# Kernel optimization log

Measured on AMD Instinct MI355X. Metric: run time of the kernel, lower is better.

## Reference

```python
import jax, jax.numpy as jnp
import numpy as np

N, D, NUM_CLASSES = 4096, 512, 128
MARGIN = 0.3


def setup_inputs() -> dict:
    key = jax.random.key(0)
    k1, k2 = jax.random.split(key)
    embeddings = jax.random.normal(k1, (N, D), dtype=jnp.float32)
    labels = jax.random.randint(k2, (N,), 0, NUM_CLASSES, dtype=jnp.int64)
    return {"embeddings": embeddings, "labels": labels}


def _batch_hard_triplet(embeddings, labels, margin):
    # L2-normalize rows (torch F.normalize: x / max(||x||, eps))
    norm = jnp.linalg.norm(embeddings, axis=1, keepdims=True)
    e = embeddings / jnp.maximum(norm, 1e-12)
    n = e.shape[0]
    # Pairwise Euclidean distance via Gram matrix; ||a-b||^2 = 2 - 2 a.b for unit vectors
    gram = e @ e.T                                   # [N, N]
    sq = jnp.clip(2.0 - 2.0 * gram, 0.0, None)
    # safe sqrt: zero (and exactly-equal) pairs get distance 0 with zero gradient
    nz = sq > 0
    dist = jnp.where(nz, jnp.sqrt(jnp.where(nz, sq, 1.0)), 0.0)  # [N, N]

    same = labels[:, None] == labels[None, :]        # [N, N] bool
    eye = jnp.eye(n, dtype=bool)
    pos_mask = same & ~eye                           # positives excluding self
    neg_mask = ~same

    # hardest positive (row max over positives), hardest negative (row min over negatives)
    dist_ap = jnp.max(jnp.where(pos_mask, dist, -jnp.inf), axis=1)  # [N]
    dist_an = jnp.min(jnp.where(neg_mask, dist, jnp.inf), axis=1)   # [N]

    valid = jnp.any(pos_mask, axis=1) & jnp.any(neg_mask, axis=1)   # rows kept by torch loop
    per_row = jax.nn.relu(dist_ap - dist_an + margin)
    num_valid = jnp.sum(valid)
    loss_sum = jnp.sum(jnp.where(valid, per_row, 0.0))
    return jnp.where(num_valid > 0, loss_sum / jnp.maximum(num_valid, 1), 0.0)


def reference(embeddings, labels):
    return _batch_hard_triplet(embeddings, labels, MARGIN)
```

## Files before the change

### kernel.cpp

```cpp
#include <hip/hip_runtime.h>
#include <hip/hip_bf16.h>
#include <stdint.h>


#define NROW 4096
#define DIM  512
#define MARGIN 0.3f
#define BT 128
#define NTILE (NROW / BT)
#define NPAIR (NTILE * (NTILE + 1) / 2)
#define POS_INIT 0xFFFFFFFFu
#define NEG_INIT 0u

typedef __attribute__((ext_vector_type(8))) __bf16 bf16x8;
typedef __attribute__((ext_vector_type(4))) float  f32x4;
typedef __attribute__((ext_vector_type(8))) unsigned short u16x8;

__device__ __forceinline__ unsigned enc(float f) {
    unsigned u = __float_as_uint(f);
    return (u & 0x80000000u) ? ~u : (u | 0x80000000u);
}
__device__ __forceinline__ float dec(unsigned e) {
    return (e & 0x80000000u) ? __uint_as_float(e & 0x7fffffffu)
                             : __uint_as_float(~e);
}

__device__ __forceinline__ unsigned short f2bf(float f) {
    __hip_bfloat16 h = __float2bfloat16(f);
    return *reinterpret_cast<unsigned short*>(&h);
}

__global__ void tl_norm(const float* __restrict__ E,
                        __hip_bfloat16* __restrict__ Ebf,
                        unsigned* __restrict__ posArr,
                        unsigned* __restrict__ negArr) {
    if (blockIdx.x < 16) {
        int t = blockIdx.x * 256 + threadIdx.x;
        posArr[t] = POS_INIT;
        negArr[t] = NEG_INIT;
    }
    const int wave  = threadIdx.x >> 6;
    const int lane  = threadIdx.x & 63;
    const int r2    = lane >> 4;
    const int kc    = lane & 15;
    const int rtile = blockIdx.x;
    const int r_in  = wave * 4 + r2;
    const int row   = rtile * 16 + r_in;

    const float4* src = (const float4*)(E + (size_t)row * DIM) + kc * 8;
    float4 v[8];
    #pragma unroll
    for (int i = 0; i < 8; i++) v[i] = src[i];

    float ss = 0.0f;
    #pragma unroll
    for (int i = 0; i < 8; i++)
        ss += v[i].x*v[i].x + v[i].y*v[i].y + v[i].z*v[i].z + v[i].w*v[i].w;
    #pragma unroll
    for (int m = 1; m < 16; m <<= 1) ss += __shfl_xor(ss, m);
    const float inv = 1.0f / fmaxf(sqrtf(ss), 1e-12f);

    u16x8* dst = (u16x8*)Ebf + (size_t)kc * 16384 + (size_t)rtile * 64 + r_in;
    #pragma unroll
    for (int c = 0; c < 4; c++) {
        const float4 lo = v[2*c], hi = v[2*c + 1];
        u16x8 o;
        o[0] = f2bf(lo.x * inv); o[1] = f2bf(lo.y * inv);
        o[2] = f2bf(lo.z * inv); o[3] = f2bf(lo.w * inv);
        o[4] = f2bf(hi.x * inv); o[5] = f2bf(hi.y * inv);
        o[6] = f2bf(hi.z * inv); o[7] = f2bf(hi.w * inv);
        dst[c * 16] = o;
    }
}

#define ISSUE8(sl, kkq) do {                                                  \
    const uint4* _pa = EaU + (size_t)(kkq) * 16384;                           \
    const uint4* _pb = EbU + (size_t)(kkq) * 16384;                           \
    asm volatile(                                                             \
        "global_load_dwordx4 %0, %8, off\n\t"                                 \
        "global_load_dwordx4 %1, %8, off offset:1024\n\t"                     \
        "global_load_dwordx4 %2, %8, off offset:2048\n\t"                     \
        "global_load_dwordx4 %3, %8, off offset:3072\n\t"                     \
        "global_load_dwordx4 %4, %9, off\n\t"                                 \
        "global_load_dwordx4 %5, %9, off offset:1024\n\t"                     \
        "global_load_dwordx4 %6, %9, off offset:2048\n\t"                     \
        "global_load_dwordx4 %7, %9, off offset:3072"                         \
        : "=&v"(a[sl][0]), "=&v"(a[sl][1]), "=&v"(a[sl][2]), "=&v"(a[sl][3]), \
          "=&v"(b[sl][0]), "=&v"(b[sl][1]), "=&v"(b[sl][2]), "=&v"(b[sl][3])  \
        : "v"(_pa), "v"(_pb));                                                \
} while (0)

#define WAITV(n) do {                                                         \
    asm volatile("s_waitcnt vmcnt(" #n ")" ::: "memory");                     \
    __builtin_amdgcn_sched_barrier(0);                                        \
} while (0)

#define MFMA16(sl) do {                                                       \
    _Pragma("unroll")                                                         \
    for (int mi = 0; mi < 4; mi++)                                            \
        _Pragma("unroll")                                                     \
        for (int ni = 0; ni < 4; ni++)                                        \
            acc[mi][ni] = __builtin_amdgcn_mfma_f32_16x16x32_bf16(            \
                a[sl][mi], b[sl][ni], acc[mi][ni], 0, 0, 0);                  \
} while (0)

__global__ void __launch_bounds__(256, 2)
tl_gram(const __hip_bfloat16* __restrict__ Ebf,
        const int* __restrict__ labels,
        unsigned* __restrict__ posArr,
        unsigned* __restrict__ negArr) {
    __shared__ int rowLab[BT];
    __shared__ int colLab[BT];

    const int bid = blockIdx.x;
    int t = (bid & 7) * (NPAIR / 8) + (bid >> 3);

    int bi = 0, rowlen = NTILE;
    while (t >= rowlen) { t -= rowlen; rowlen--; bi++; }
    const int bj = bi + t;

    const int tid  = threadIdx.x;
    const int wave = tid >> 6;
    const int lane = tid & 63;
    const int quad = lane >> 4;
    const int l16  = lane & 15;
    const int wr   = wave >> 1;
    const int wc   = wave & 1;
    const int tileI = bi * BT;
    const int tileJ = bj * BT;
    const bool diag = (bi == bj);

    if (tid < BT) rowLab[tid] = labels[tileI + tid];
    else          colLab[tid - BT] = labels[tileJ + (tid - BT)];
    __syncthreads();

    const uint4* Ev  = (const uint4*)Ebf;
    const uint4* EaU = Ev + ((tileI + wr * 64) >> 4) * 64 + lane;
    const uint4* EbU = Ev + ((tileJ + wc * 64) >> 4) * 64 + lane;

    f32x4 acc[4][4] = {};
    bf16x8 a[4][4], b[4][4];

    ISSUE8(0, 0); ISSUE8(1, 1); ISSUE8(2, 2);

    ISSUE8(3, 3);   WAITV(24); MFMA16(0);
    ISSUE8(0, 4);   WAITV(24); MFMA16(1);
    ISSUE8(1, 5);   WAITV(24); MFMA16(2);
    ISSUE8(2, 6);   WAITV(24); MFMA16(3);
    ISSUE8(3, 7);   WAITV(24); MFMA16(0);
    ISSUE8(0, 8);   WAITV(24); MFMA16(1);
    ISSUE8(1, 9);   WAITV(24); MFMA16(2);
    ISSUE8(2, 10);  WAITV(24); MFMA16(3);
    ISSUE8(3, 11);  WAITV(24); MFMA16(0);
    ISSUE8(0, 12);  WAITV(24); MFMA16(1);
    ISSUE8(1, 13);  WAITV(24); MFMA16(2);
    ISSUE8(2, 14);  WAITV(24); MFMA16(3);
    ISSUE8(3, 15);  WAITV(24); MFMA16(0);
                    WAITV(16); MFMA16(1);
                    WAITV(8);  MFMA16(2);
                    WAITV(0);  MFMA16(3);

    int rl[16], cl[4], clocv[4];
    #pragma unroll
    for (int mi = 0; mi < 4; mi++)
        #pragma unroll
        for (int reg = 0; reg < 4; reg++)
            rl[mi * 4 + reg] = rowLab[wr * 64 + mi * 16 + quad * 4 + reg];
    #pragma unroll
    for (int ni = 0; ni < 4; ni++) {
        clocv[ni] = wc * 64 + ni * 16 + l16;
        cl[ni] = colLab[clocv[ni]];
    }

    #pragma unroll
    for (int mi = 0; mi < 4; mi++) {
        #pragma unroll
        for (int reg = 0; reg < 4; reg++) {
            const int rloc = wr * 64 + mi * 16 + quad * 4 + reg;
            const int lr   = rl[mi * 4 + reg];
            const int gi   = tileI + rloc;
            float pmin =  INFINITY;
            float nmax = -INFINITY;
            #pragma unroll
            for (int ni = 0; ni < 4; ni++) {
                const int gj  = tileJ + clocv[ni];
                const float g = acc[mi][ni][reg];
                const bool same = (lr == cl[ni]);
                if (same && gi != gj) pmin = fminf(pmin, g);
                if (!same)            nmax = fmaxf(nmax, g);
            }
            #pragma unroll
            for (int m = 1; m < 16; m <<= 1) {
                pmin = fminf(pmin, __shfl_xor(pmin, m));
                nmax = fmaxf(nmax, __shfl_xor(nmax, m));
            }
            if (l16 == 0) {
                if (pmin <  INFINITY) atomicMin(&posArr[gi], enc(pmin));
                if (nmax > -INFINITY) atomicMax(&negArr[gi], enc(nmax));
            }
        }
    }

    if (!diag) {
        #pragma unroll
        for (int ni = 0; ni < 4; ni++) {
            const int lc = cl[ni];
            const int gj = tileJ + clocv[ni];
            float pmin =  INFINITY;
            float nmax = -INFINITY;
            #pragma unroll
            for (int mi = 0; mi < 4; mi++) {
                #pragma unroll
                for (int reg = 0; reg < 4; reg++) {
                    const float g = acc[mi][ni][reg];
                    const bool same = (rl[mi * 4 + reg] == lc);
                    if (same) pmin = fminf(pmin, g);
                    else      nmax = fmaxf(nmax, g);
                }
            }
            pmin = fminf(pmin, __shfl_xor(pmin, 16));
            pmin = fminf(pmin, __shfl_xor(pmin, 32));
            nmax = fmaxf(nmax, __shfl_xor(nmax, 16));
            nmax = fmaxf(nmax, __shfl_xor(nmax, 32));
            if (quad == 0) {
                if (pmin <  INFINITY) atomicMin(&posArr[gj], enc(pmin));
                if (nmax > -INFINITY) atomicMax(&negArr[gj], enc(nmax));
            }
        }
    }
}

__global__ void tl_final(const unsigned* __restrict__ posArr,
                         const unsigned* __restrict__ negArr,
                         float* __restrict__ out) {
    const int tid = threadIdx.x;
    uint4 pe4 = ((const uint4*)posArr)[tid];
    uint4 ne4 = ((const uint4*)negArr)[tid];
    unsigned pes[4] = {pe4.x, pe4.y, pe4.z, pe4.w};
    unsigned nes[4] = {ne4.x, ne4.y, ne4.z, ne4.w};
    float sum = 0.0f;
    int   count = 0;
    #pragma unroll
    for (int j = 0; j < 4; j++) {
        const bool valid = (pes[j] != POS_INIT) && (nes[j] != NEG_INIT);
        const float dap = sqrtf(fmaxf(2.0f - 2.0f * dec(pes[j]), 0.0f));
        const float dan = sqrtf(fmaxf(2.0f - 2.0f * dec(nes[j]), 0.0f));
        const float per = fmaxf(dap - dan + MARGIN, 0.0f);
        if (valid) { sum += per; count += 1; }
    }
    #pragma unroll
    for (int m = 32; m >= 1; m >>= 1) {
        sum   += __shfl_xor(sum, m);
        count += __shfl_xor(count, m);
    }
    __shared__ float ssum[16];
    __shared__ int   scnt[16];
    const int wave = tid >> 6, lane = tid & 63;
    if (lane == 0) { ssum[wave] = sum; scnt[wave] = count; }
    __syncthreads();
    if (tid == 0) {
        float s = 0.0f; int c = 0;
        #pragma unroll
        for (int w = 0; w < 16; w++) { s += ssum[w]; c += scnt[w]; }
        out[0] = (c > 0) ? (s / (float)c) : 0.0f;
    }
}

extern "C" void kernel_launch(void* const* d_in, const int* in_sizes, int n_in,
                              void* d_out, int out_size, void* d_ws, size_t ws_size,
                              hipStream_t stream) {
    const float* E      = (const float*)d_in[0];
    const int*   labels = (const int*)d_in[1];
    float*       out    = (float*)d_out;

    char* ws = (char*)d_ws;
    __hip_bfloat16* Ebf   = (__hip_bfloat16*)ws;
    unsigned* posArr      = (unsigned*)(ws + (size_t)NROW * DIM * 2);
    unsigned* negArr      = posArr + NROW;

    tl_norm<<<NROW / 16, 256, 0, stream>>>(E, Ebf, posArr, negArr);
    tl_gram<<<NPAIR, 256, 0, stream>>>(Ebf, labels, posArr, negArr);
    tl_final<<<1, 1024, 0, stream>>>(posArr, negArr, out);
}
```

Baseline: 94.98 us.

## Stage Gram operand tiles through LDS via async global-to-LDS loads

Replaces the per-wave direct global-to-register loads with a block-cooperative global_load_lds copy into a 4-stage shared-memory ring. Each K-slice of the row and column tiles is loaded once per block and read by waves with ds_read_b128. This removes the duplicate global loads where waves sharing a row or column tile each fetched it, and it frees the VGPRs that held prefetched operands. In exchange it adds two block barriers per K step and LDS read latency before each MFMA group.

```diff
diff --git a/kernel.cpp b/kernel.cpp
--- a/kernel.cpp
+++ b/kernel.cpp
@@ -30,6 +30,13 @@
     return *reinterpret_cast<unsigned short*>(&h);
 }
 
+__device__ __forceinline__ void async_copy16(const void* g, void* l) {
+    __builtin_amdgcn_global_load_lds(
+        (const __attribute__((address_space(1))) unsigned int*)g,
+        (__attribute__((address_space(3))) unsigned int*)l,
+        16, 0, 0);
+}
+
 __global__ void tl_norm(const float* __restrict__ E,
                         __hip_bfloat16* __restrict__ Ebf,
                         unsigned* __restrict__ posArr,
@@ -73,21 +80,18 @@
     }
 }
 
-#define ISSUE8(sl, kkq) do {                                                  \
-    const uint4* _pa = EaU + (size_t)(kkq) * 16384;                           \
-    const uint4* _pb = EbU + (size_t)(kkq) * 16384;                           \
-    asm volatile(                                                             \
-        "global_load_dwordx4 %0, %8, off\n\t"                                 \
-        "global_load_dwordx4 %1, %8, off offset:1024\n\t"                     \
-        "global_load_dwordx4 %2, %8, off offset:2048\n\t"                     \
-        "global_load_dwordx4 %3, %8, off offset:3072\n\t"                     \
-        "global_load_dwordx4 %4, %9, off\n\t"                                 \
-        "global_load_dwordx4 %5, %9, off offset:1024\n\t"                     \
-        "global_load_dwordx4 %6, %9, off offset:2048\n\t"                     \
-        "global_load_dwordx4 %7, %9, off offset:3072"                         \
-        : "=&v"(a[sl][0]), "=&v"(a[sl][1]), "=&v"(a[sl][2]), "=&v"(a[sl][3]), \
-          "=&v"(b[sl][0]), "=&v"(b[sl][1]), "=&v"(b[sl][2]), "=&v"(b[sl][3])  \
-        : "v"(_pa), "v"(_pb));                                                \
+#define ISSUE(s) do {                                                         \
+    if ((s) < 16) {                                                           \
+        _Pragma("unroll")                                                     \
+        for (int q = 0; q < 4; ++q) {                                         \
+            const int c   = wave * 4 + q;                                     \
+            const int rt0 = (c >= 8) ? rtJ0 : rtI0;                           \
+            const int rt  = (c >= 8) ? c - 8 : c;                             \
+            const uint4* src = Ev + (size_t)(s) * 16384                       \
+                                  + (size_t)(rt0 + rt) * 64 + lane;           \
+            async_copy16(src, &sbuf[(s) & 3][c][0]);                          \
+        }                                                                     \
+    }                                                                         \
 } while (0)
 
 #define WAITV(n) do {                                                         \
@@ -95,13 +99,34 @@
     __builtin_amdgcn_sched_barrier(0);                                        \
 } while (0)
 
-#define MFMA16(sl) do {                                                       \
+#define DSR(dst, addr) \
+    asm volatile("ds_read_b128 %0, %1" : "=&v"(dst) : "v"(addr));
+
+#define COMPUTE(s) do {                                                       \
+    bf16x8 af[4], bg[4];                                                      \
+    _Pragma("unroll")                                                         \
+    for (int mi = 0; mi < 4; mi++)                                            \
+        DSR(af[mi], vA + (unsigned)(((s) & 3) * 16384 + mi * 1024));          \
+    _Pragma("unroll")                                                         \
+    for (int ni = 0; ni < 4; ni++)                                            \
+        DSR(bg[ni], vB + (unsigned)(((s) & 3) * 16384 + ni * 1024));          \
+    asm volatile("s_waitcnt lgkmcnt(0)" ::: "memory");                        \
+    __builtin_amdgcn_sched_barrier(0);                                        \
     _Pragma("unroll")                                                         \
     for (int mi = 0; mi < 4; mi++)                                            \
         _Pragma("unroll")                                                     \
         for (int ni = 0; ni < 4; ni++)                                        \
             acc[mi][ni] = __builtin_amdgcn_mfma_f32_16x16x32_bf16(            \
-                a[sl][mi], b[sl][ni], acc[mi][ni], 0, 0, 0);                  \
+                af[mi], bg[ni], acc[mi][ni], 0, 0, 0);                        \
+} while (0)
+
+#define STEP(s, w) do {                                                       \
+    WAITV(w);                                                                 \
+    __builtin_amdgcn_s_barrier();                                             \
+    COMPUTE(s);                                                               \
+    __builtin_amdgcn_sched_barrier(0);                                        \
+    __builtin_amdgcn_s_barrier();                                             \
+    ISSUE((s) + 4);                                                           \
 } while (0)
 
 __global__ void __launch_bounds__(256, 2)
@@ -109,6 +134,7 @@
         const int* __restrict__ labels,
         unsigned* __restrict__ posArr,
         unsigned* __restrict__ negArr) {
+    __shared__ uint4 sbuf[4][16][64];
     __shared__ int rowLab[BT];
     __shared__ int colLab[BT];
 
@@ -134,31 +160,23 @@
     else          colLab[tid - BT] = labels[tileJ + (tid - BT)];
     __syncthreads();
 
-    const uint4* Ev  = (const uint4*)Ebf;
-    const uint4* EaU = Ev + ((tileI + wr * 64) >> 4) * 64 + lane;
-    const uint4* EbU = Ev + ((tileJ + wc * 64) >> 4) * 64 + lane;
+    const int rtI0 = tileI >> 4;
+    const int rtJ0 = tileJ >> 4;
+    const uint4* Ev = (const uint4*)Ebf;
+
+    const uint32_t sbase =
+        (uint32_t)(uintptr_t)(__attribute__((address_space(3))) void*)&sbuf[0][0][0];
+    const uint32_t vA = sbase + (uint32_t)(wr * 4 * 1024) + (uint32_t)(lane * 16);
+    const uint32_t vB = sbase + (uint32_t)((8 + wc * 4) * 1024) + (uint32_t)(lane * 16);
 
     f32x4 acc[4][4] = {};
-    bf16x8 a[4][4], b[4][4];
-
-    ISSUE8(0, 0); ISSUE8(1, 1); ISSUE8(2, 2);
-
-    ISSUE8(3, 3);   WAITV(24); MFMA16(0);
-    ISSUE8(0, 4);   WAITV(24); MFMA16(1);
-    ISSUE8(1, 5);   WAITV(24); MFMA16(2);
-    ISSUE8(2, 6);   WAITV(24); MFMA16(3);
-    ISSUE8(3, 7);   WAITV(24); MFMA16(0);
-    ISSUE8(0, 8);   WAITV(24); MFMA16(1);
-    ISSUE8(1, 9);   WAITV(24); MFMA16(2);
-    ISSUE8(2, 10);  WAITV(24); MFMA16(3);
-    ISSUE8(3, 11);  WAITV(24); MFMA16(0);
-    ISSUE8(0, 12);  WAITV(24); MFMA16(1);
-    ISSUE8(1, 13);  WAITV(24); MFMA16(2);
-    ISSUE8(2, 14);  WAITV(24); MFMA16(3);
-    ISSUE8(3, 15);  WAITV(24); MFMA16(0);
-                    WAITV(16); MFMA16(1);
-                    WAITV(8);  MFMA16(2);
-                    WAITV(0);  MFMA16(3);
+
+    ISSUE(0); ISSUE(1); ISSUE(2); ISSUE(3);
+
+    STEP(0, 12);  STEP(1, 12);  STEP(2, 12);  STEP(3, 12);
+    STEP(4, 12);  STEP(5, 12);  STEP(6, 12);  STEP(7, 12);
+    STEP(8, 12);  STEP(9, 12);  STEP(10, 12); STEP(11, 12);
+    STEP(12, 12); STEP(13, 8);  STEP(14, 4);  STEP(15, 0);
 
     int rl[16], cl[4], clocv[4];
     #pragma unroll
```

After: 93.13 us. No clear change (-1.9%).
